# Kernel optimization log

Hardware: AMD Instinct MI355X
Metric: run time of the kernel (lower is better)

## Reference

```python
import jax, jax.numpy as jnp
import numpy as np

T, DIM, AH, HID, E = 2048, 1024, 2048, 1024, 8
N_HEADS, HEAD_DIM = 16, 128
N_GROUPS, TOPK_GROUPS, TOPK = 4, 2, 1
ROUTE_SCALE = 1.0


def rmsnorm(x, w, eps=1e-6):
    xf = x.astype(jnp.float32)
    var = jnp.mean(xf * xf, axis=-1, keepdims=True)
    return (xf * jax.lax.rsqrt(var + eps)).astype(x.dtype) * w


def setup_inputs() -> dict:
    key = jax.random.key(0)
    ks = jax.random.split(key, 12)

    def xavier(k, fan_in, fan_out, gain=1.0):
        lim = gain * np.sqrt(6.0 / (fan_in + fan_out))
        return jax.random.uniform(k, (fan_in, fan_out), minval=-lim, maxval=lim, dtype=jnp.float32)

    return {
        "x": jax.random.normal(ks[0], (T, DIM), dtype=jnp.float32),
        "x_projected": jax.random.normal(ks[1], (T, AH), dtype=jnp.float32),
        "attn_norm_w": jnp.ones((AH,), dtype=jnp.float32),
        # stored as [in, out] (transposed vs torch Linear)
        "wq": 0.02 * jax.random.normal(ks[2], (AH, N_HEADS * HEAD_DIM), dtype=jnp.float32),
        "bq": jnp.zeros((N_HEADS * HEAD_DIM,), dtype=jnp.float32),
        "wk": 0.02 * jax.random.normal(ks[3], (AH, N_HEADS * HEAD_DIM), dtype=jnp.float32),
        "bk": jnp.zeros((N_HEADS * HEAD_DIM,), dtype=jnp.float32),
        "q_norm_w": jnp.ones((HEAD_DIM,), dtype=jnp.float32),
        "k_norm_w": jnp.ones((HEAD_DIM,), dtype=jnp.float32),
        "w1": xavier(ks[4], DIM, HID),
        "b1": jnp.zeros((HID,), dtype=jnp.float32),
        "w2": xavier(ks[5], HID, HID),
        "b2": jnp.zeros((HID,), dtype=jnp.float32),
        "w3": xavier(ks[6], HID, E, gain=0.1),
        "b3": jnp.zeros((E,), dtype=jnp.float32),
    }


def reference(x, x_projected, attn_norm_w, wq, bq, wk, bk, q_norm_w, k_norm_w,
              w1, b1, w2, b2, w3, b3):
    t = x.shape[0]
    # ---- attention probe (torch.no_grad -> stop_gradient) ----
    xn = rmsnorm(x_projected, attn_norm_w)                      # [T, AH]
    q = (xn @ wq + bq).reshape(t, N_HEADS, HEAD_DIM)
    k = (xn @ wk + bk).reshape(t, N_HEADS, HEAD_DIM)
    q = rmsnorm(q, q_norm_w)
    k = rmsnorm(k, k_norm_w)
    scores = jnp.einsum('qhd,khd->hqk', q, k) / np.float32(np.sqrt(HEAD_DIM))
    probs = jax.nn.softmax(scores, axis=-1)                     # [H, T, T]
    # sum over query axis, mean over heads -> attention received per token
    importance = jax.lax.stop_gradient(probs.sum(axis=1).mean(axis=0))  # [T]

    # ---- router MLP (eval mode: dropout = identity) ----
    h = jax.nn.gelu(x @ w1 + b1, approximate=False)
    h = jax.nn.gelu(h @ w2 + b2, approximate=False)
    logits = h @ w3 + b3                                        # [T, E]
    r_scores = jax.nn.softmax(logits, axis=-1)

    # ---- grouped top-k (group-limited top-1 routing) ----
    sg = r_scores.reshape(t, N_GROUPS, E // N_GROUPS)
    group_scores = sg.max(axis=-1)                              # [T, G]
    _, gidx = jax.lax.top_k(group_scores, TOPK_GROUPS)          # [T, kg]
    mask = jnp.zeros((t, N_GROUPS), dtype=bool).at[jnp.arange(t)[:, None], gidx].set(True)
    masked = jnp.where(mask[:, :, None], sg, -jnp.inf).reshape(t, E)
    _, idx = jax.lax.top_k(masked, TOPK)                        # [T, 1]
    weights = jnp.take_along_axis(r_scores, idx, axis=1) * ROUTE_SCALE  # [T, 1]
    return weights, idx, importance
```

## Files before the change

### kernel.cpp

```cpp
#include <hip/hip_runtime.h>

#define T_TOK 2048
#define DIMX  1024
#define AHX   2048
#define HIDX  1024
#define NEXP  8
#define NHEAD 16
#define HD    128

typedef unsigned short us;
typedef short bf16x8 __attribute__((ext_vector_type(8)));
typedef float f32x4  __attribute__((ext_vector_type(4)));

__device__ __forceinline__ us f2bf(float f){
  unsigned int u = __builtin_bit_cast(unsigned int, f);
  u += 0x7FFFu + ((u >> 16) & 1u);
  return (us)(u >> 16);
}
__device__ __forceinline__ float bf2f(us h){
  unsigned int u = ((unsigned int)h) << 16;
  return __builtin_bit_cast(float, u);
}
__device__ __forceinline__ float gelu_exact(float x){
  return 0.5f * x * (1.0f + erff(x * 0.70710678118654752440f));
}
__device__ __forceinline__ void gload16(const us* g, us* l){
  __builtin_amdgcn_global_load_lds((const __attribute__((address_space(1))) unsigned int*)g,
                                   (__attribute__((address_space(3))) unsigned int*)l, 16, 0, 0);
}

__global__ __launch_bounds__(256) void k_pre(const float* __restrict__ x,
                                             us* __restrict__ xh, us* __restrict__ xl,
                                             const float* __restrict__ xproj,
                                             const float* __restrict__ anw,
                                             us* __restrict__ xn,
                                             const float* __restrict__ wq,
                                             const float* __restrict__ wk,
                                             us* __restrict__ wqkT,
                                             const float* __restrict__ w1,
                                             const float* __restrict__ w2,
                                             us* __restrict__ w1h, us* __restrict__ w1l,
                                             us* __restrict__ w2h, us* __restrict__ w2l){
  __shared__ float tile[32][33];
  __shared__ float ps[4];
  int bx = blockIdx.x, t = threadIdx.x;
  if (bx < 8192){
    int i = bx * 256 + t;
    float v = x[i];
    us h = f2bf(v);
    xh[i] = h;
    xl[i] = f2bf(v - bf2f(h));
    return;
  }
  if (bx < 10240){
    int row = bx - 8192;
    const float* p = xproj + (size_t)row * AHX;
    float v[8];
    *(float4*)&v[0] = *(const float4*)(p + t * 8);
    *(float4*)&v[4] = *(const float4*)(p + t * 8 + 4);
    float s = 0.f;
    #pragma unroll
    for (int i = 0; i < 8; i++) s += v[i] * v[i];
    #pragma unroll
    for (int m = 1; m < 64; m <<= 1) s += __shfl_xor(s, m);
    if ((t & 63) == 0) ps[t >> 6] = s;
    __syncthreads();
    float tot = ps[0] + ps[1] + ps[2] + ps[3];
    float rs = rsqrtf(tot * (1.0f / AHX) + 1e-6f);
    #pragma unroll
    for (int i = 0; i < 8; i++)
      xn[(size_t)row * AHX + t * 8 + i] = f2bf(v[i] * rs * anw[t * 8 + i]);
    return;
  }
  int tx = t & 31, ty = t >> 5;
  if (bx < 18432){
    int sub = bx - 10240;
    const float* in = (sub >> 12) ? wk : wq;
    us* o = wqkT + (size_t)(sub >> 12) * AHX * AHX;
    int rem = sub & 4095;
    int tbx = (rem & 63) * 32, tby = (rem >> 6) * 32;
    #pragma unroll
    for (int i = 0; i < 32; i += 8)
      tile[ty + i][tx] = in[(size_t)(tby + ty + i) * AHX + tbx + tx];
    __syncthreads();
    #pragma unroll
    for (int i = 0; i < 32; i += 8)
      o[(size_t)(tbx + ty + i) * AHX + tby + tx] = f2bf(tile[tx][ty + i]);
    return;
  }
  {
    int sub = bx - 18432;
    const float* in = (sub >> 10) ? w2 : w1;
    us* oh = (sub >> 10) ? w2h : w1h;
    us* ol = (sub >> 10) ? w2l : w1l;
    int rem = sub & 1023;
    int tbx = (rem & 31) * 32, tby = (rem >> 5) * 32;
    #pragma unroll
    for (int i = 0; i < 32; i += 8)
      tile[ty + i][tx] = in[(size_t)(tby + ty + i) * HIDX + tbx + tx];
    __syncthreads();
    #pragma unroll
    for (int i = 0; i < 32; i += 8){
      float v = tile[tx][ty + i];
      us h = f2bf(v);
      size_t o = (size_t)(tbx + ty + i) * DIMX + tby + tx;
      oh[o] = h;
      ol[o] = f2bf(v - bf2f(h));
    }
  }
}

__global__ __launch_bounds__(512) void k_gemm_qk(
    const us* __restrict__ A, const us* __restrict__ B,
    const float* __restrict__ bq, const float* __restrict__ bk,
    const float* __restrict__ qnw, const float* __restrict__ knw,
    us* __restrict__ Qnn, us* __restrict__ Knn, int K)
{
  __shared__ __align__(16) us sA[2][128 * 64];
  __shared__ __align__(16) us sB[2][128 * 64];
  __shared__ float sums[128][4];
  int tid = threadIdx.x;
  int bm = blockIdx.y * 128;
  int bnB = blockIdx.x * 128;
  int w = tid >> 6, l = tid & 63;
  int wm = (w >> 2) * 64, wn = (w & 3) * 32;
  int lhi = l >> 4, llo = l & 15;
  int srow = l >> 3;
  int scol = ((l & 7) ^ srow) * 8;
  int swz = llo & 7;

  const us* pA = &A[(size_t)(bm + w * 16 + srow) * K + scol];
  const us* pB = &B[(size_t)(bnB + w * 16 + srow) * K + scol];

  f32x4 acc[4][2] = {};

  #pragma unroll
  for (int i = 0; i < 2; i++){
    gload16(pA + (size_t)i * 8 * K, &sA[0][(w * 16 + i * 8) * 64]);
    gload16(pB + (size_t)i * 8 * K, &sB[0][(w * 16 + i * 8) * 64]);
  }
  __syncthreads();

  int cur = 0;
  for (int k0 = 0; k0 < K; k0 += 64){
    if (k0 + 64 < K){
      #pragma unroll
      for (int i = 0; i < 2; i++){
        gload16(pA + (size_t)i * 8 * K + k0 + 64, &sA[cur ^ 1][(w * 16 + i * 8) * 64]);
        gload16(pB + (size_t)i * 8 * K + k0 + 64, &sB[cur ^ 1][(w * 16 + i * 8) * 64]);
      }
    }
    bf16x8 af[2][4], bfr[2][2];
    #pragma unroll
    for (int kk = 0; kk < 2; kk++){
      int ca = ((kk * 4 + lhi) ^ swz) * 8;
      #pragma unroll
      for (int m = 0; m < 4; m++)
        af[kk][m] = *(const bf16x8*)&sA[cur][(wm + m * 16 + llo) * 64 + ca];
      #pragma unroll
      for (int n = 0; n < 2; n++)
        bfr[kk][n] = *(const bf16x8*)&sB[cur][(wn + n * 16 + llo) * 64 + ca];
    }
    #pragma unroll
    for (int kk = 0; kk < 2; kk++)
      #pragma unroll
      for (int m = 0; m < 4; m++)
        #pragma unroll
        for (int n = 0; n < 2; n++)
          acc[m][n] = __builtin_amdgcn_mfma_f32_16x16x32_bf16(af[kk][m], bfr[kk][n], acc[m][n], 0, 0, 0);
    __syncthreads();
    cur ^= 1;
  }

  bool isq = blockIdx.x < 16;
  const float* bias = isq ? bq : bk;
  const float* nw   = isq ? qnw : knw;
  us* outp = isq ? Qnn : Knn;
  int hcol0 = (blockIdx.x & 15) * 128;

  #pragma unroll
  for (int n = 0; n < 2; n++){
    float bv = bias[hcol0 + wn + n * 16 + llo];
    #pragma unroll
    for (int m = 0; m < 4; m++)
      #pragma unroll
      for (int j = 0; j < 4; j++) acc[m][n][j] += bv;
  }
  #pragma unroll
  for (int m = 0; m < 4; m++)
    #pragma unroll
    for (int j = 0; j < 4; j++){
      float p = 0.f;
      #pragma unroll
      for (int n = 0; n < 2; n++) p += acc[m][n][j] * acc[m][n][j];
      p += __shfl_xor(p, 1); p += __shfl_xor(p, 2);
      p += __shfl_xor(p, 4); p += __shfl_xor(p, 8);
      if (llo == 0) sums[wm + m * 16 + lhi * 4 + j][w & 3] = p;
    }
  __syncthreads();
  #pragma unroll
  for (int m = 0; m < 4; m++)
    #pragma unroll
    for (int j = 0; j < 4; j++){
      int row = wm + m * 16 + lhi * 4 + j;
      float rs = rsqrtf((sums[row][0] + sums[row][1] + sums[row][2] + sums[row][3]) * (1.0f / HD) + 1e-6f);
      #pragma unroll
      for (int n = 0; n < 2; n++){
        int col = wn + n * 16 + llo;
        outp[(size_t)(bm + row) * AHX + hcol0 + col] = f2bf(acc[m][n][j] * rs * nw[col]);
      }
    }
}

template<int EPI>
__global__ __launch_bounds__(256) void k_gemm_mlp(
    const us* __restrict__ Ah_, const us* __restrict__ Al_,
    const us* __restrict__ Bh_, const us* __restrict__ Bl_,
    const float* __restrict__ bias,
    float* __restrict__ Cf, us* __restrict__ Ch, us* __restrict__ Cl,
    int N, int K)
{
  __shared__ __align__(16) us sAh[2][64 * 64], sAl[2][64 * 64];
  __shared__ __align__(16) us sBh[2][64 * 64], sBl[2][64 * 64];
  int tid = threadIdx.x;
  int bm = blockIdx.y * 64, bn = blockIdx.x * 64;
  int w = tid >> 6, l = tid & 63;
  int wm = (w >> 1) * 32, wn = (w & 1) * 32;
  int lhi = l >> 4, llo = l & 15;
  int srow = l >> 3;
  int scol = ((l & 7) ^ srow) * 8;
  int swz = llo & 7;

  const us* pAh = &Ah_[(size_t)(bm + w * 8 + srow) * K + scol];
  const us* pAl = &Al_[(size_t)(bm + w * 8 + srow) * K + scol];
  const us* pBh = &Bh_[(size_t)(bn + w * 8 + srow) * K + scol];
  const us* pBl = &Bl_[(size_t)(bn + w * 8 + srow) * K + scol];

  f32x4 acc[2][2] = {};

  auto stage = [&](int buf, int k0){
    #pragma unroll
    for (int i = 0; i < 2; i++){
      int rb = (i * 32 + w * 8) * 64;
      gload16(pAh + (size_t)i * 32 * K + k0, &sAh[buf][rb]);
      gload16(pAl + (size_t)i * 32 * K + k0, &sAl[buf][rb]);
      gload16(pBh + (size_t)i * 32 * K + k0, &sBh[buf][rb]);
      gload16(pBl + (size_t)i * 32 * K + k0, &sBl[buf][rb]);
    }
  };

  stage(0, 0);
  __syncthreads();

  int cur = 0;
  for (int k0 = 0; k0 < K; k0 += 64){
    if (k0 + 64 < K) stage(cur ^ 1, k0 + 64);
    bf16x8 ah[2][2], al[2][2], bh[2][2], bl[2][2];
    #pragma unroll
    for (int kk = 0; kk < 2; kk++){
      int ca = ((kk * 4 + lhi) ^ swz) * 8;
      #pragma unroll
      for (int m = 0; m < 2; m++){
        ah[kk][m] = *(const bf16x8*)&sAh[cur][(wm + m * 16 + llo) * 64 + ca];
        al[kk][m] = *(const bf16x8*)&sAl[cur][(wm + m * 16 + llo) * 64 + ca];
        bh[kk][m] = *(const bf16x8*)&sBh[cur][(wn + m * 16 + llo) * 64 + ca];
        bl[kk][m] = *(const bf16x8*)&sBl[cur][(wn + m * 16 + llo) * 64 + ca];
      }
    }
    #pragma unroll
    for (int kk = 0; kk < 2; kk++)
      #pragma unroll
      for (int m = 0; m < 2; m++)
        #pragma unroll
        for (int n = 0; n < 2; n++){
          acc[m][n] = __builtin_amdgcn_mfma_f32_16x16x32_bf16(ah[kk][m], bh[kk][n], acc[m][n], 0, 0, 0);
          acc[m][n] = __builtin_amdgcn_mfma_f32_16x16x32_bf16(ah[kk][m], bl[kk][n], acc[m][n], 0, 0, 0);
          acc[m][n] = __builtin_amdgcn_mfma_f32_16x16x32_bf16(al[kk][m], bh[kk][n], acc[m][n], 0, 0, 0);
        }
    __syncthreads();
    cur ^= 1;
  }

  #pragma unroll
  for (int m = 0; m < 2; m++)
    #pragma unroll
    for (int n = 0; n < 2; n++){
      int col = bn + wn + n * 16 + llo;
      float bv = bias[col];
      #pragma unroll
      for (int j = 0; j < 4; j++){
        int row = bm + wm + m * 16 + lhi * 4 + j;
        float v = acc[m][n][j] + bv;
        size_t off = (size_t)row * N + col;
        if constexpr (EPI == 1){
          float g = gelu_exact(v);
          us hh = f2bf(g);
          Ch[off] = hh;
          Cl[off] = f2bf(g - bf2f(hh));
        } else {
          Cf[off] = gelu_exact(v);
        }
      }
    }
}

__global__ __launch_bounds__(512) void k_z(const us* __restrict__ Qn,
                                           const us* __restrict__ Kn,
                                           float* __restrict__ zpart){
  __shared__ __align__(16) us sK[2][128 * 128];
  int h = blockIdx.y;
  int qb = blockIdx.x * 256;
  int tid = threadIdx.x, w = tid >> 6, l = tid & 63;
  int lhi = l >> 4, llo = l & 15;
  int wq = qb + w * 32;
  const float scale = 0.08838834764831845f;

  auto stageK = [&](int buf, int kt){
    #pragma unroll
    for (int i = 0; i < 4; i++){
      int rb = w * 16 + i * 4;
      int r = rb + lhi;
      int c = (llo ^ (r & 7)) * 8;
      gload16(&Kn[(size_t)(kt + r) * AHX + h * HD + c], &sK[buf][rb * 128]);
    }
  };

  bf16x8 qf[2][4];
  #pragma unroll
  for (int m = 0; m < 2; m++)
    #pragma unroll
    for (int kk = 0; kk < 4; kk++)
      qf[m][kk] = *(const bf16x8*)&Qn[(size_t)(wq + m * 16 + llo) * AHX + h * HD + kk * 32 + lhi * 8];

  float rz[2][4] = {};
  int kt0 = blockIdx.z * 512;

  stageK(0, kt0);
  __syncthreads();

  #pragma unroll
  for (int t = 0; t < 4; t++){
    int cur = t & 1;
    if (t + 1 < 4) stageK(cur ^ 1, kt0 + (t + 1) * 128);
    f32x4 acc[2][8] = {};
    #pragma unroll
    for (int n = 0; n < 8; n++){
      int row = n * 16 + llo;
      #pragma unroll
      for (int kk = 0; kk < 4; kk++){
        bf16x8 kf = *(const bf16x8*)&sK[cur][row * 128 + ((kk * 32 + lhi * 8) ^ ((llo & 7) << 3))];
        acc[0][n] = __builtin_amdgcn_mfma_f32_16x16x32_bf16(qf[0][kk], kf, acc[0][n], 0, 0, 0);
        acc[1][n] = __builtin_amdgcn_mfma_f32_16x16x32_bf16(qf[1][kk], kf, acc[1][n], 0, 0, 0);
      }
    }
    #pragma unroll
    for (int m = 0; m < 2; m++)
      #pragma unroll
      for (int j = 0; j < 4; j++){
        float s = 0.f;
        #pragma unroll
        for (int n = 0; n < 8; n++) s += __expf(acc[m][n][j] * scale);
        rz[m][j] += s;
      }
    if (t + 1 < 4) __syncthreads();
  }
  #pragma unroll
  for (int m = 0; m < 2; m++)
    #pragma unroll
    for (int j = 0; j < 4; j++){
      float s = rz[m][j];
      s += __shfl_xor(s, 1); s += __shfl_xor(s, 2);
      s += __shfl_xor(s, 4); s += __shfl_xor(s, 8);
      if (llo == 0){
        int row = wq + m * 16 + lhi * 4 + j;
        zpart[(size_t)blockIdx.z * (NHEAD * T_TOK) + h * T_TOK + row] = s;
      }
    }
}

__global__ __launch_bounds__(512) void k_imp(const us* __restrict__ Qn,
                                             const us* __restrict__ Kn,
                                             const float* __restrict__ zpart,
                                             float* __restrict__ imp_part){
  __shared__ __align__(16) us sK[2][128 * 128];
  __shared__ float simp[8][128];
  int h = blockIdx.y;
  int qb = blockIdx.x * 256;
  int kt0 = blockIdx.z * 512;
  int tid = threadIdx.x, w = tid >> 6, l = tid & 63;
  int lhi = l >> 4, llo = l & 15;
  int wq = qb + w * 32;
  const float scale = 0.08838834764831845f;

  auto stageK = [&](int buf, int kt){
    #pragma unroll
    for (int i = 0; i < 4; i++){
      int rb = w * 16 + i * 4;
      int r = rb + lhi;
      int c = (llo ^ (r & 7)) * 8;
      gload16(&Kn[(size_t)(kt + r) * AHX + h * HD + c], &sK[buf][rb * 128]);
    }
  };

  bf16x8 qf[2][4];
  float rcv[2][4];
  #pragma unroll
  for (int m = 0; m < 2; m++)
    #pragma unroll
    for (int kk = 0; kk < 4; kk++)
      qf[m][kk] = *(const bf16x8*)&Qn[(size_t)(wq + m * 16 + llo) * AHX + h * HD + kk * 32 + lhi * 8];
  #pragma unroll
  for (int m = 0; m < 2; m++)
    #pragma unroll
    for (int j = 0; j < 4; j++){
      int row = wq + m * 16 + lhi * 4 + j;
      float zs = 0.f;
      #pragma unroll
      for (int p = 0; p < 4; p++) zs += zpart[(size_t)p * (NHEAD * T_TOK) + h * T_TOK + row];
      rcv[m][j] = 1.0f / ((float)NHEAD * zs);
    }

  stageK(0, kt0);
  __syncthreads();

  #pragma unroll
  for (int t = 0; t < 4; t++){
    int cur = t & 1;
    if (t + 1 < 4) stageK(cur ^ 1, kt0 + (t + 1) * 128);
    f32x4 acc[2][8] = {};
    #pragma unroll
    for (int n = 0; n < 8; n++){
      int row = n * 16 + llo;
      #pragma unroll
      for (int kk = 0; kk < 4; kk++){
        bf16x8 kf = *(const bf16x8*)&sK[cur][row * 128 + ((kk * 32 + lhi * 8) ^ ((llo & 7) << 3))];
        acc[0][n] = __builtin_amdgcn_mfma_f32_16x16x32_bf16(qf[0][kk], kf, acc[0][n], 0, 0, 0);
        acc[1][n] = __builtin_amdgcn_mfma_f32_16x16x32_bf16(qf[1][kk], kf, acc[1][n], 0, 0, 0);
      }
    }
    #pragma unroll
    for (int n = 0; n < 8; n++){
      float s = 0.f;
      #pragma unroll
      for (int m = 0; m < 2; m++)
        #pragma unroll
        for (int j = 0; j < 4; j++)
          s += __expf(acc[m][n][j] * scale) * rcv[m][j];
      s += __shfl_xor(s, 16);
      s += __shfl_xor(s, 32);
      if (l < 16) simp[w][n * 16 + l] = s;
    }
    __syncthreads();
    if (tid < 128){
      float tot = 0.f;
      #pragma unroll
      for (int ww = 0; ww < 8; ww++) tot += simp[ww][tid];
      imp_part[((size_t)blockIdx.x * NHEAD + h) * T_TOK + kt0 + t * 128 + tid] = tot;
    }
    __syncthreads();
  }
}

__global__ __launch_bounds__(256) void k_final(const float* __restrict__ imp_part,
                                               const float* __restrict__ h2,
                                               const float* __restrict__ w3,
                                               const float* __restrict__ b3,
                                               float* __restrict__ out){
  if (blockIdx.x < 8){
    int col = blockIdx.x * 256 + threadIdx.x;
    float s = 0.f;
    for (int r = 0; r < 128; r++) s += imp_part[(size_t)r * T_TOK + col];
    out[2 * T_TOK + col] = s;
    return;
  }
  int t = (blockIdx.x - 8) * 4 + (threadIdx.x >> 6);
  int l = threadIdx.x & 63;
  const float* hp = h2 + (size_t)t * HIDX;
  float acc[NEXP] = {};
  for (int i = l; i < HIDX; i += 64){
    float hv = hp[i];
    const float* wr = w3 + (size_t)i * NEXP;
    #pragma unroll
    for (int e = 0; e < NEXP; e++) acc[e] = fmaf(hv, wr[e], acc[e]);
  }
  #pragma unroll
  for (int mk = 1; mk < 64; mk <<= 1)
    #pragma unroll
    for (int e = 0; e < NEXP; e++) acc[e] += __shfl_xor(acc[e], mk);
  if (l == 0){
    float lg[NEXP], mx = -__builtin_inff();
    #pragma unroll
    for (int e = 0; e < NEXP; e++){ lg[e] = acc[e] + b3[e]; mx = fmaxf(mx, lg[e]); }
    float Z = 0.f, p[NEXP];
    #pragma unroll
    for (int e = 0; e < NEXP; e++){ p[e] = expf(lg[e] - mx); Z += p[e]; }
    float invZ = 1.0f / Z;
    #pragma unroll
    for (int e = 0; e < NEXP; e++) p[e] *= invZ;
    float gs[4];
    #pragma unroll
    for (int g = 0; g < 4; g++) gs[g] = fmaxf(p[2 * g], p[2 * g + 1]);
    int g1 = 0;
    #pragma unroll
    for (int g = 1; g < 4; g++) if (gs[g] > gs[g1]) g1 = g;
    int g2 = -1; float g2v = -__builtin_inff();
    #pragma unroll
    for (int g = 0; g < 4; g++) if (g != g1 && gs[g] > g2v){ g2v = gs[g]; g2 = g; }
    int best = 0; float bv = -__builtin_inff();
    #pragma unroll
    for (int e = 0; e < NEXP; e++){
      int g = e >> 1;
      if ((g == g1 || g == g2) && p[e] > bv){ bv = p[e]; best = e; }
    }
    out[t]         = bv;
    out[T_TOK + t] = (float)best;
  }
}

extern "C" void kernel_launch(void* const* d_in, const int* in_sizes, int n_in,
                              void* d_out, int out_size, void* d_ws, size_t ws_size,
                              hipStream_t stream){
  const float* x     = (const float*)d_in[0];
  const float* xproj = (const float*)d_in[1];
  const float* anw   = (const float*)d_in[2];
  const float* wq    = (const float*)d_in[3];
  const float* bq    = (const float*)d_in[4];
  const float* wk    = (const float*)d_in[5];
  const float* bk    = (const float*)d_in[6];
  const float* qnw   = (const float*)d_in[7];
  const float* knw   = (const float*)d_in[8];
  const float* w1    = (const float*)d_in[9];
  const float* b1    = (const float*)d_in[10];
  const float* w2    = (const float*)d_in[11];
  const float* b2    = (const float*)d_in[12];
  const float* w3    = (const float*)d_in[13];
  const float* b3    = (const float*)d_in[14];
  float* out = (float*)d_out;

  char* ws = (char*)d_ws;
  const size_t MB = 1024 * 1024;
  us* xn      = (us*)(ws);
  us* wqkT    = (us*)(ws + 8 * MB);
  us* Qnn     = (us*)(ws + 24 * MB);
  us* Knn     = (us*)(ws + 32 * MB);
  float* zpart    = (float*)(ws + 40 * MB);
  float* imp_part = (float*)(ws + 42 * MB);
  us* xh      = (us*)(ws + 44 * MB);
  us* xl      = (us*)(ws + 48 * MB);
  us* w1Th    = (us*)(ws + 52 * MB);
  us* w1Tl    = (us*)(ws + 54 * MB);
  us* w2Th    = (us*)(ws + 56 * MB);
  us* w2Tl    = (us*)(ws + 58 * MB);
  us* h1h     = (us*)(ws + 60 * MB);
  us* h1l     = (us*)(ws + 64 * MB);
  float* h2   = (float*)(ws + 68 * MB);

  k_pre<<<20480, 256, 0, stream>>>(x, xh, xl, xproj, anw, xn,
                                   wq, wk, wqkT, w1, w2, w1Th, w1Tl, w2Th, w2Tl);

  k_gemm_qk<<<dim3(32, 16), 512, 0, stream>>>(xn, wqkT, bq, bk, qnw, knw, Qnn, Knn, AHX);

  k_z<<<dim3(8, NHEAD, 4), 512, 0, stream>>>(Qnn, Knn, zpart);
  k_imp<<<dim3(8, NHEAD, 4), 512, 0, stream>>>(Qnn, Knn, zpart, imp_part);

  k_gemm_mlp<1><<<dim3(HIDX / 64, T_TOK / 64), 256, 0, stream>>>(
      xh, xl, w1Th, w1Tl, b1, nullptr, h1h, h1l, HIDX, DIMX);
  k_gemm_mlp<2><<<dim3(HIDX / 64, T_TOK / 64), 256, 0, stream>>>(
      h1h, h1l, w2Th, w2Tl, b2, h2, nullptr, nullptr, HIDX, HIDX);

  k_final<<<8 + T_TOK / 4, 256, 0, stream>>>(imp_part, h2, w3, b3, out);

  (void)in_sizes; (void)n_in; (void)out_size; (void)ws_size;
}
```

Measured before the change: 213.9 us.

## Widen QK GEMM tile and split attention score kernels into per-K-tile blocks

```diff
diff --git a/kernel.cpp b/kernel.cpp
--- a/kernel.cpp
+++ b/kernel.cpp
@@ -117,70 +117,73 @@
     us* __restrict__ Qnn, us* __restrict__ Knn, int K)
 {
   __shared__ __align__(16) us sA[2][128 * 64];
-  __shared__ __align__(16) us sB[2][128 * 64];
-  __shared__ float sums[128][4];
+  __shared__ __align__(16) us sB[2][256 * 64];
+  __shared__ float sums[128][2][2];
   int tid = threadIdx.x;
   int bm = blockIdx.y * 128;
-  int bnB = blockIdx.x * 128;
+  int bnB = blockIdx.x * 256;
   int w = tid >> 6, l = tid & 63;
-  int wm = (w >> 2) * 64, wn = (w & 3) * 32;
+  int wm = (w >> 2) * 64, wn = (w & 3) * 64;
   int lhi = l >> 4, llo = l & 15;
   int srow = l >> 3;
   int scol = ((l & 7) ^ srow) * 8;
   int swz = llo & 7;
 
   const us* pA = &A[(size_t)(bm + w * 16 + srow) * K + scol];
-  const us* pB = &B[(size_t)(bnB + w * 16 + srow) * K + scol];
-
-  f32x4 acc[4][2] = {};
-
-  #pragma unroll
-  for (int i = 0; i < 2; i++){
+  const us* pB = &B[(size_t)(bnB + w * 32 + srow) * K + scol];
+
+  f32x4 acc[4][4] = {};
+
+  #pragma unroll
+  for (int i = 0; i < 2; i++)
     gload16(pA + (size_t)i * 8 * K, &sA[0][(w * 16 + i * 8) * 64]);
-    gload16(pB + (size_t)i * 8 * K, &sB[0][(w * 16 + i * 8) * 64]);
-  }
+  #pragma unroll
+  for (int i = 0; i < 4; i++)
+    gload16(pB + (size_t)i * 8 * K, &sB[0][(w * 32 + i * 8) * 64]);
   __syncthreads();
 
   int cur = 0;
   for (int k0 = 0; k0 < K; k0 += 64){
     if (k0 + 64 < K){
       #pragma unroll
-      for (int i = 0; i < 2; i++){
+      for (int i = 0; i < 2; i++)
         gload16(pA + (size_t)i * 8 * K + k0 + 64, &sA[cur ^ 1][(w * 16 + i * 8) * 64]);
-        gload16(pB + (size_t)i * 8 * K + k0 + 64, &sB[cur ^ 1][(w * 16 + i * 8) * 64]);
-      }
-    }
-    bf16x8 af[2][4], bfr[2][2];
+      #pragma unroll
+      for (int i = 0; i < 4; i++)
+        gload16(pB + (size_t)i * 8 * K + k0 + 64, &sB[cur ^ 1][(w * 32 + i * 8) * 64]);
+    }
+    bf16x8 af[2][4], bfr[2][4];
     #pragma unroll
     for (int kk = 0; kk < 2; kk++){
       int ca = ((kk * 4 + lhi) ^ swz) * 8;
       #pragma unroll
-      for (int m = 0; m < 4; m++)
-        af[kk][m] = *(const bf16x8*)&sA[cur][(wm + m * 16 + llo) * 64 + ca];
-      #pragma unroll
-      for (int n = 0; n < 2; n++)
-        bfr[kk][n] = *(const bf16x8*)&sB[cur][(wn + n * 16 + llo) * 64 + ca];
+      for (int m = 0; m < 4; m++){
+        af[kk][m]  = *(const bf16x8*)&sA[cur][(wm + m * 16 + llo) * 64 + ca];
+        bfr[kk][m] = *(const bf16x8*)&sB[cur][(wn + m * 16 + llo) * 64 + ca];
+      }
     }
     #pragma unroll
     for (int kk = 0; kk < 2; kk++)
       #pragma unroll
       for (int m = 0; m < 4; m++)
         #pragma unroll
-        for (int n = 0; n < 2; n++)
+        for (int n = 0; n < 4; n++)
           acc[m][n] = __builtin_amdgcn_mfma_f32_16x16x32_bf16(af[kk][m], bfr[kk][n], acc[m][n], 0, 0, 0);
     __syncthreads();
     cur ^= 1;
   }
 
-  bool isq = blockIdx.x < 16;
+  bool isq = blockIdx.x < 8;
   const float* bias = isq ? bq : bk;
   const float* nw   = isq ? qnw : knw;
   us* outp = isq ? Qnn : Knn;
-  int hcol0 = (blockIdx.x & 15) * 128;
-
-  #pragma unroll
-  for (int n = 0; n < 2; n++){
-    float bv = bias[hcol0 + wn + n * 16 + llo];
+  int hbase = bnB & 2047;
+  int hc = wn >> 7;
+  int widx = (wn >> 6) & 1;
+
+  #pragma unroll
+  for (int n = 0; n < 4; n++){
+    float bv = bias[hbase + wn + n * 16 + llo];
     #pragma unroll
     for (int m = 0; m < 4; m++)
       #pragma unroll
@@ -192,10 +195,10 @@
     for (int j = 0; j < 4; j++){
       float p = 0.f;
       #pragma unroll
-      for (int n = 0; n < 2; n++) p += acc[m][n][j] * acc[m][n][j];
+      for (int n = 0; n < 4; n++) p += acc[m][n][j] * acc[m][n][j];
       p += __shfl_xor(p, 1); p += __shfl_xor(p, 2);
       p += __shfl_xor(p, 4); p += __shfl_xor(p, 8);
-      if (llo == 0) sums[wm + m * 16 + lhi * 4 + j][w & 3] = p;
+      if (llo == 0) sums[wm + m * 16 + lhi * 4 + j][hc][widx] = p;
     }
   __syncthreads();
   #pragma unroll
@@ -203,11 +206,11 @@
     #pragma unroll
     for (int j = 0; j < 4; j++){
       int row = wm + m * 16 + lhi * 4 + j;
-      float rs = rsqrtf((sums[row][0] + sums[row][1] + sums[row][2] + sums[row][3]) * (1.0f / HD) + 1e-6f);
-      #pragma unroll
-      for (int n = 0; n < 2; n++){
-        int col = wn + n * 16 + llo;
-        outp[(size_t)(bm + row) * AHX + hcol0 + col] = f2bf(acc[m][n][j] * rs * nw[col]);
+      float rs = rsqrtf((sums[row][hc][0] + sums[row][hc][1]) * (1.0f / HD) + 1e-6f);
+      #pragma unroll
+      for (int n = 0; n < 4; n++){
+        int colblk = wn + n * 16 + llo;
+        outp[(size_t)(bm + row) * AHX + hbase + colblk] = f2bf(acc[m][n][j] * rs * nw[colblk & 127]);
       }
     }
 }
@@ -304,26 +307,31 @@
     }
 }
 
+__device__ __forceinline__ void score_decode(int d, int& qb_i, int& h, int& zc){
+  int glo = d & 7, qb = (d >> 3) & 7, ghi = d >> 6;
+  int g = ghi * 8 + glo;
+  h = g & 15; zc = g >> 4; qb_i = qb;
+}
+
 __global__ __launch_bounds__(512) void k_z(const us* __restrict__ Qn,
                                            const us* __restrict__ Kn,
                                            float* __restrict__ zpart){
-  __shared__ __align__(16) us sK[2][128 * 128];
-  int h = blockIdx.y;
-  int qb = blockIdx.x * 256;
+  __shared__ __align__(16) us sK[128 * 128];
+  int qb_i, h, zc;
+  score_decode(blockIdx.x, qb_i, h, zc);
   int tid = threadIdx.x, w = tid >> 6, l = tid & 63;
   int lhi = l >> 4, llo = l & 15;
-  int wq = qb + w * 32;
+  int wq = qb_i * 256 + w * 32;
+  int kt = zc * 128;
   const float scale = 0.08838834764831845f;
 
-  auto stageK = [&](int buf, int kt){
-    #pragma unroll
-    for (int i = 0; i < 4; i++){
-      int rb = w * 16 + i * 4;
-      int r = rb + lhi;
-      int c = (llo ^ (r & 7)) * 8;
-      gload16(&Kn[(size_t)(kt + r) * AHX + h * HD + c], &sK[buf][rb * 128]);
-    }
-  };
+  #pragma unroll
+  for (int i = 0; i < 4; i++){
+    int rb = w * 16 + i * 4;
+    int r = rb + lhi;
+    int c = (llo ^ (r & 7)) * 8;
+    gload16(&Kn[(size_t)(kt + r) * AHX + h * HD + c], &sK[rb * 128]);
+  }
 
   bf16x8 qf[2][4];
   #pragma unroll
@@ -331,49 +339,31 @@
     #pragma unroll
     for (int kk = 0; kk < 4; kk++)
       qf[m][kk] = *(const bf16x8*)&Qn[(size_t)(wq + m * 16 + llo) * AHX + h * HD + kk * 32 + lhi * 8];
-
-  float rz[2][4] = {};
-  int kt0 = blockIdx.z * 512;
-
-  stageK(0, kt0);
   __syncthreads();
 
-  #pragma unroll
-  for (int t = 0; t < 4; t++){
-    int cur = t & 1;
-    if (t + 1 < 4) stageK(cur ^ 1, kt0 + (t + 1) * 128);
-    f32x4 acc[2][8] = {};
-    #pragma unroll
-    for (int n = 0; n < 8; n++){
-      int row = n * 16 + llo;
-      #pragma unroll
-      for (int kk = 0; kk < 4; kk++){
-        bf16x8 kf = *(const bf16x8*)&sK[cur][row * 128 + ((kk * 32 + lhi * 8) ^ ((llo & 7) << 3))];
-        acc[0][n] = __builtin_amdgcn_mfma_f32_16x16x32_bf16(qf[0][kk], kf, acc[0][n], 0, 0, 0);
-        acc[1][n] = __builtin_amdgcn_mfma_f32_16x16x32_bf16(qf[1][kk], kf, acc[1][n], 0, 0, 0);
-      }
-    }
-    #pragma unroll
-    for (int m = 0; m < 2; m++)
-      #pragma unroll
-      for (int j = 0; j < 4; j++){
-        float s = 0.f;
-        #pragma unroll
-        for (int n = 0; n < 8; n++) s += __expf(acc[m][n][j] * scale);
-        rz[m][j] += s;
-      }
-    if (t + 1 < 4) __syncthreads();
+  f32x4 acc[2][8] = {};
+  #pragma unroll
+  for (int n = 0; n < 8; n++){
+    int row = n * 16 + llo;
+    #pragma unroll
+    for (int kk = 0; kk < 4; kk++){
+      bf16x8 kf = *(const bf16x8*)&sK[row * 128 + ((kk * 32 + lhi * 8) ^ ((llo & 7) << 3))];
+      acc[0][n] = __builtin_amdgcn_mfma_f32_16x16x32_bf16(qf[0][kk], kf, acc[0][n], 0, 0, 0);
+      acc[1][n] = __builtin_amdgcn_mfma_f32_16x16x32_bf16(qf[1][kk], kf, acc[1][n], 0, 0, 0);
+    }
   }
   #pragma unroll
   for (int m = 0; m < 2; m++)
     #pragma unroll
     for (int j = 0; j < 4; j++){
-      float s = rz[m][j];
+      float s = 0.f;
+      #pragma unroll
+      for (int n = 0; n < 8; n++) s += __expf(acc[m][n][j] * scale);
       s += __shfl_xor(s, 1); s += __shfl_xor(s, 2);
       s += __shfl_xor(s, 4); s += __shfl_xor(s, 8);
       if (llo == 0){
         int row = wq + m * 16 + lhi * 4 + j;
-        zpart[(size_t)blockIdx.z * (NHEAD * T_TOK) + h * T_TOK + row] = s;
+        zpart[(size_t)zc * (NHEAD * T_TOK) + h * T_TOK + row] = s;
       }
     }
 }
@@ -382,25 +372,23 @@
                                              const us* __restrict__ Kn,
                                              const float* __restrict__ zpart,
                                              float* __restrict__ imp_part){
-  __shared__ __align__(16) us sK[2][128 * 128];
+  __shared__ __align__(16) us sK[128 * 128];
   __shared__ float simp[8][128];
-  int h = blockIdx.y;
-  int qb = blockIdx.x * 256;
-  int kt0 = blockIdx.z * 512;
+  int qb_i, h, zc;
+  score_decode(blockIdx.x, qb_i, h, zc);
   int tid = threadIdx.x, w = tid >> 6, l = tid & 63;
   int lhi = l >> 4, llo = l & 15;
-  int wq = qb + w * 32;
+  int wq = qb_i * 256 + w * 32;
+  int kt = zc * 128;
   const float scale = 0.08838834764831845f;
 
-  auto stageK = [&](int buf, int kt){
-    #pragma unroll
-    for (int i = 0; i < 4; i++){
-      int rb = w * 16 + i * 4;
-      int r = rb + lhi;
-      int c = (llo ^ (r & 7)) * 8;
-      gload16(&Kn[(size_t)(kt + r) * AHX + h * HD + c], &sK[buf][rb * 128]);
-    }
-  };
+  #pragma unroll
+  for (int i = 0; i < 4; i++){
+    int rb = w * 16 + i * 4;
+    int r = rb + lhi;
+    int c = (llo ^ (r & 7)) * 8;
+    gload16(&Kn[(size_t)(kt + r) * AHX + h * HD + c], &sK[rb * 128]);
+  }
 
   bf16x8 qf[2][4];
   float rcv[2][4];
@@ -416,48 +404,40 @@
       int row = wq + m * 16 + lhi * 4 + j;
       float zs = 0.f;
       #pragma unroll
-      for (int p = 0; p < 4; p++) zs += zpart[(size_t)p * (NHEAD * T_TOK) + h * T_TOK + row];
+      for (int p = 0; p < 16; p++) zs += zpart[(size_t)p * (NHEAD * T_TOK) + h * T_TOK + row];
       rcv[m][j] = 1.0f / ((float)NHEAD * zs);
     }
-
-  stageK(0, kt0);
   __syncthreads();
 
-  #pragma unroll
-  for (int t = 0; t < 4; t++){
-    int cur = t & 1;
-    if (t + 1 < 4) stageK(cur ^ 1, kt0 + (t + 1) * 128);
-    f32x4 acc[2][8] = {};
-    #pragma unroll
-    for (int n = 0; n < 8; n++){
-      int row = n * 16 + llo;
-      #pragma unroll
-      for (int kk = 0; kk < 4; kk++){
-        bf16x8 kf = *(const bf16x8*)&sK[cur][row * 128 + ((kk * 32 + lhi * 8) ^ ((llo & 7) << 3))];
-        acc[0][n] = __builtin_amdgcn_mfma_f32_16x16x32_bf16(qf[0][kk], kf, acc[0][n], 0, 0, 0);
-        acc[1][n] = __builtin_amdgcn_mfma_f32_16x16x32_bf16(qf[1][kk], kf, acc[1][n], 0, 0, 0);
-      }
-    }
-    #pragma unroll
-    for (int n = 0; n < 8; n++){
-      float s = 0.f;
-      #pragma unroll
-      for (int m = 0; m < 2; m++)
-        #pragma unroll
-        for (int j = 0; j < 4; j++)
-          s += __expf(acc[m][n][j] * scale) * rcv[m][j];
-      s += __shfl_xor(s, 16);
-      s += __shfl_xor(s, 32);
-      if (l < 16) simp[w][n * 16 + l] = s;
-    }
-    __syncthreads();
-    if (tid < 128){
-      float tot = 0.f;
-      #pragma unroll
-      for (int ww = 0; ww < 8; ww++) tot += simp[ww][tid];
-      imp_part[((size_t)blockIdx.x * NHEAD + h) * T_TOK + kt0 + t * 128 + tid] = tot;
-    }
-    __syncthreads();
+  f32x4 acc[2][8] = {};
+  #pragma unroll
+  for (int n = 0; n < 8; n++){
+    int row = n * 16 + llo;
+    #pragma unroll
+    for (int kk = 0; kk < 4; kk++){
+      bf16x8 kf = *(const bf16x8*)&sK[row * 128 + ((kk * 32 + lhi * 8) ^ ((llo & 7) << 3))];
+      acc[0][n] = __builtin_amdgcn_mfma_f32_16x16x32_bf16(qf[0][kk], kf, acc[0][n], 0, 0, 0);
+      acc[1][n] = __builtin_amdgcn_mfma_f32_16x16x32_bf16(qf[1][kk], kf, acc[1][n], 0, 0, 0);
+    }
+  }
+  #pragma unroll
+  for (int n = 0; n < 8; n++){
+    float s = 0.f;
+    #pragma unroll
+    for (int m = 0; m < 2; m++)
+      #pragma unroll
+      for (int j = 0; j < 4; j++)
+        s += __expf(acc[m][n][j] * scale) * rcv[m][j];
+    s += __shfl_xor(s, 16);
+    s += __shfl_xor(s, 32);
+    if (l < 16) simp[w][n * 16 + l] = s;
+  }
+  __syncthreads();
+  if (tid < 128){
+    float tot = 0.f;
+    #pragma unroll
+    for (int ww = 0; ww < 8; ww++) tot += simp[ww][tid];
+    imp_part[((size_t)qb_i * NHEAD + h) * T_TOK + kt + tid] = tot;
   }
 }
 
@@ -558,10 +538,10 @@
   k_pre<<<20480, 256, 0, stream>>>(x, xh, xl, xproj, anw, xn,
                                    wq, wk, wqkT, w1, w2, w1Th, w1Tl, w2Th, w2Tl);
 
-  k_gemm_qk<<<dim3(32, 16), 512, 0, stream>>>(xn, wqkT, bq, bk, qnw, knw, Qnn, Knn, AHX);
-
-  k_z<<<dim3(8, NHEAD, 4), 512, 0, stream>>>(Qnn, Knn, zpart);
-  k_imp<<<dim3(8, NHEAD, 4), 512, 0, stream>>>(Qnn, Knn, zpart, imp_part);
+  k_gemm_qk<<<dim3(16, 16), 512, 0, stream>>>(xn, wqkT, bq, bk, qnw, knw, Qnn, Knn, AHX);
+
+  k_z<<<2048, 512, 0, stream>>>(Qnn, Knn, zpart);
+  k_imp<<<2048, 512, 0, stream>>>(Qnn, Knn, zpart, imp_part);
 
   k_gemm_mlp<1><<<dim3(HIDX / 64, T_TOK / 64), 256, 0, stream>>>(
       xh, xl, w1Th, w1Tl, b1, nullptr, h1h, h1l, HIDX, DIMX);
```

New measurement: 219.2 us. 2.5% more time.

## Split attention score kernels over 8 key chunks with XCD-aware block mapping

Applied to the files above, without the earlier changes.

```diff
diff --git a/kernel.cpp b/kernel.cpp
--- a/kernel.cpp
+++ b/kernel.cpp
@@ -304,15 +304,22 @@
     }
 }
 
+__device__ __forceinline__ void score_decode(int d, int& qb_i, int& h, int& zc){
+  int glo = d & 7, qb = (d >> 3) & 7, ghi = d >> 6;
+  int g = ghi * 8 + glo;
+  h = g & 15; zc = g >> 4; qb_i = qb;
+}
+
 __global__ __launch_bounds__(512) void k_z(const us* __restrict__ Qn,
                                            const us* __restrict__ Kn,
                                            float* __restrict__ zpart){
   __shared__ __align__(16) us sK[2][128 * 128];
-  int h = blockIdx.y;
-  int qb = blockIdx.x * 256;
+  int qb_i, h, zc;
+  score_decode(blockIdx.x, qb_i, h, zc);
   int tid = threadIdx.x, w = tid >> 6, l = tid & 63;
   int lhi = l >> 4, llo = l & 15;
-  int wq = qb + w * 32;
+  int wq = qb_i * 256 + w * 32;
+  int kt0 = zc * 256;
   const float scale = 0.08838834764831845f;
 
   auto stageK = [&](int buf, int kt){
@@ -333,22 +340,20 @@
       qf[m][kk] = *(const bf16x8*)&Qn[(size_t)(wq + m * 16 + llo) * AHX + h * HD + kk * 32 + lhi * 8];
 
   float rz[2][4] = {};
-  int kt0 = blockIdx.z * 512;
 
   stageK(0, kt0);
   __syncthreads();
 
   #pragma unroll
-  for (int t = 0; t < 4; t++){
-    int cur = t & 1;
-    if (t + 1 < 4) stageK(cur ^ 1, kt0 + (t + 1) * 128);
+  for (int t = 0; t < 2; t++){
+    if (t == 0) stageK(1, kt0 + 128);
     f32x4 acc[2][8] = {};
     #pragma unroll
     for (int n = 0; n < 8; n++){
       int row = n * 16 + llo;
       #pragma unroll
       for (int kk = 0; kk < 4; kk++){
-        bf16x8 kf = *(const bf16x8*)&sK[cur][row * 128 + ((kk * 32 + lhi * 8) ^ ((llo & 7) << 3))];
+        bf16x8 kf = *(const bf16x8*)&sK[t][row * 128 + ((kk * 32 + lhi * 8) ^ ((llo & 7) << 3))];
         acc[0][n] = __builtin_amdgcn_mfma_f32_16x16x32_bf16(qf[0][kk], kf, acc[0][n], 0, 0, 0);
         acc[1][n] = __builtin_amdgcn_mfma_f32_16x16x32_bf16(qf[1][kk], kf, acc[1][n], 0, 0, 0);
       }
@@ -362,7 +367,7 @@
         for (int n = 0; n < 8; n++) s += __expf(acc[m][n][j] * scale);
         rz[m][j] += s;
       }
-    if (t + 1 < 4) __syncthreads();
+    if (t == 0) __syncthreads();
   }
   #pragma unroll
   for (int m = 0; m < 2; m++)
@@ -373,7 +378,7 @@
       s += __shfl_xor(s, 4); s += __shfl_xor(s, 8);
       if (llo == 0){
         int row = wq + m * 16 + lhi * 4 + j;
-        zpart[(size_t)blockIdx.z * (NHEAD * T_TOK) + h * T_TOK + row] = s;
+        zpart[((size_t)h * T_TOK + row) * 8 + zc] = s;
       }
     }
 }
@@ -384,12 +389,12 @@
                                              float* __restrict__ imp_part){
   __shared__ __align__(16) us sK[2][128 * 128];
   __shared__ float simp[8][128];
-  int h = blockIdx.y;
-  int qb = blockIdx.x * 256;
-  int kt0 = blockIdx.z * 512;
+  int qb_i, h, zc;
+  score_decode(blockIdx.x, qb_i, h, zc);
   int tid = threadIdx.x, w = tid >> 6, l = tid & 63;
   int lhi = l >> 4, llo = l & 15;
-  int wq = qb + w * 32;
+  int wq = qb_i * 256 + w * 32;
+  int kt0 = zc * 256;
   const float scale = 0.08838834764831845f;
 
   auto stageK = [&](int buf, int kt){
@@ -414,9 +419,9 @@
     #pragma unroll
     for (int j = 0; j < 4; j++){
       int row = wq + m * 16 + lhi * 4 + j;
-      float zs = 0.f;
-      #pragma unroll
-      for (int p = 0; p < 4; p++) zs += zpart[(size_t)p * (NHEAD * T_TOK) + h * T_TOK + row];
+      const float4* zp4 = (const float4*)&zpart[((size_t)h * T_TOK + row) * 8];
+      float4 a = zp4[0], b = zp4[1];
+      float zs = a.x + a.y + a.z + a.w + b.x + b.y + b.z + b.w;
       rcv[m][j] = 1.0f / ((float)NHEAD * zs);
     }
 
@@ -424,16 +429,15 @@
   __syncthreads();
 
   #pragma unroll
-  for (int t = 0; t < 4; t++){
-    int cur = t & 1;
-    if (t + 1 < 4) stageK(cur ^ 1, kt0 + (t + 1) * 128);
+  for (int t = 0; t < 2; t++){
+    if (t == 0) stageK(1, kt0 + 128);
     f32x4 acc[2][8] = {};
     #pragma unroll
     for (int n = 0; n < 8; n++){
       int row = n * 16 + llo;
       #pragma unroll
       for (int kk = 0; kk < 4; kk++){
-        bf16x8 kf = *(const bf16x8*)&sK[cur][row * 128 + ((kk * 32 + lhi * 8) ^ ((llo & 7) << 3))];
+        bf16x8 kf = *(const bf16x8*)&sK[t][row * 128 + ((kk * 32 + lhi * 8) ^ ((llo & 7) << 3))];
         acc[0][n] = __builtin_amdgcn_mfma_f32_16x16x32_bf16(qf[0][kk], kf, acc[0][n], 0, 0, 0);
         acc[1][n] = __builtin_amdgcn_mfma_f32_16x16x32_bf16(qf[1][kk], kf, acc[1][n], 0, 0, 0);
       }
@@ -455,7 +459,7 @@
       float tot = 0.f;
       #pragma unroll
       for (int ww = 0; ww < 8; ww++) tot += simp[ww][tid];
-      imp_part[((size_t)blockIdx.x * NHEAD + h) * T_TOK + kt0 + t * 128 + tid] = tot;
+      imp_part[((size_t)qb_i * NHEAD + h) * T_TOK + kt0 + t * 128 + tid] = tot;
     }
     __syncthreads();
   }
@@ -560,8 +564,8 @@
 
   k_gemm_qk<<<dim3(32, 16), 512, 0, stream>>>(xn, wqkT, bq, bk, qnw, knw, Qnn, Knn, AHX);
 
-  k_z<<<dim3(8, NHEAD, 4), 512, 0, stream>>>(Qnn, Knn, zpart);
-  k_imp<<<dim3(8, NHEAD, 4), 512, 0, stream>>>(Qnn, Knn, zpart, imp_part);
+  k_z<<<1024, 512, 0, stream>>>(Qnn, Knn, zpart);
+  k_imp<<<1024, 512, 0, stream>>>(Qnn, Knn, zpart, imp_part);
 
   k_gemm_mlp<1><<<dim3(HIDX / 64, T_TOK / 64), 256, 0, stream>>>(
       xh, xl, w1Th, w1Tl, b1, nullptr, h1h, h1l, HIDX, DIMX);
```

After: 190.9 us. -10.7%, faster.
